# Kernel optimization log

Measured on AMD Instinct MI355X. Metric: run time of the kernel, lower is better.

## Reference

```python
import jax, jax.numpy as jnp
import numpy as np

TMP1 = 0.01
TMP2 = 0.1
TMP3 = 0.1
NEG_MARGIN = 0.1  # referenced in source forward but never set in __init__; fixed here
CLAMP_MAX = 88.0


def setup_inputs() -> dict:
    key = jax.random.key(0)
    scores = jax.random.normal(key, (512, 8192), dtype=jnp.float32)
    k_vals = jnp.array([1, 5, 10], dtype=jnp.int32)
    return {"scores": scores, "k_vals": k_vals, "pos_num": 16}


def reference(scores, k_vals, pos_num):
    # scores: [B, N]; first `pos_num` columns are positives (gt == 1), rest negatives.
    P = pos_num
    K = k_vals.shape[0]
    pos = scores[:, :P]          # [B, P]
    neg = scores[:, P:]          # [B, N-P]

    # pairwise diffs: pos rows and neg rows of the per-sample [N, P] diff matrix
    pos_diff = pos[:, :, None] - pos[:, None, :]                    # [B, P, P]
    neg_diff = neg[:, :, None] - pos[:, None, :] + NEG_MARGIN       # [B, N-P, P]

    # negative rows: soft step via temperature-scaled softplus, two-sided
    neg_term = jnp.where(
        neg_diff >= 0,
        jnp.logaddexp(0.0, neg_diff / TMP2) + 0.1,
        jnp.logaddexp(0.0, neg_diff / TMP1),
    )                                                               # [B, N-P, P]

    # positive rows: hard indicator (detached in source), zero the diagonal
    eye = jnp.eye(P, dtype=scores.dtype)
    pos_term = (pos_diff >= 0).astype(scores.dtype) * (1.0 - eye)   # [B, P, P]

    # soft rank of each positive: 1 + sum over all rows
    rank = 1.0 + pos_term.sum(axis=1) + neg_term.sum(axis=1)        # [B, P]

    # soft recall@k penalty per positive and cutoff
    z = (rank[:, :, None] - k_vals[None, None, :].astype(scores.dtype)) / TMP3
    recall = jnp.logaddexp(0.0, jnp.minimum(z, CLAMP_MAX))          # [B, P, K]

    per_sample = recall.sum(axis=(1, 2)) / (P * K)                  # [B]
    return per_sample.mean()
```

## Files before the change

### kernel.cpp

```cpp
#include <hip/hip_runtime.h>


#define ROWS 512
#define COLS 8192
#define POSN 16
#define NK 3
#define NEGF4 2044
#define BLOCK 512

typedef float f32x4 __attribute__((ext_vector_type(4)));

__global__ __launch_bounds__(BLOCK, 4)
void recall_fused_kernel(const float* __restrict__ scores,
                         const int* __restrict__ k_vals,
                         float* __restrict__ out)
{
    const int row  = blockIdx.x;
    const int tid  = threadIdx.x;
    const int wave = tid >> 6;
    const int lane = tid & 63;
    const float* rowp = scores + (size_t)row * COLS;

    __shared__ float s_pos[POSN];
    __shared__ float s_part[8][POSN];

    if (tid < POSN) s_pos[tid] = rowp[tid];
    __syncthreads();

    const float C10 = 14.4269504089f;
    const float A0  = 1.44269504089f;
    const float LN2 = 0.69314718055994531f;

    float p10[POSN];
#pragma unroll
    for (int j = 0; j < POSN; ++j) p10[j] = s_pos[j] * C10;

    float prod[POSN], accM[POSN];
    int   ncnt[POSN];
#pragma unroll
    for (int j = 0; j < POSN; ++j) { prod[j] = 1.0f; accM[j] = 0.0f; ncnt[j] = 0; }

    const f32x4* negs = reinterpret_cast<const f32x4*>(rowp + POSN);

    f32x4 v[4];
#pragma unroll
    for (int it = 0; it < 4; ++it) {
        int f = it * BLOCK + tid;
        if (it == 3 && f >= NEGF4) f = NEGF4 - 1;
        v[it] = __builtin_nontemporal_load(negs + f);
    }
    if (3 * BLOCK + tid >= NEGF4) {
        v[3].x = -1.0e30f; v[3].y = -1.0e30f; v[3].z = -1.0e30f; v[3].w = -1.0e30f;
    }

#pragma unroll
    for (int it = 0; it < 4; ++it) {
        float a10[4];
        a10[0] = __fmaf_rn(v[it].x, C10, A0);
        a10[1] = __fmaf_rn(v[it].y, C10, A0);
        a10[2] = __fmaf_rn(v[it].z, C10, A0);
        a10[3] = __fmaf_rn(v[it].w, C10, A0);
#pragma unroll
        for (int e = 0; e < 4; ++e) {
#pragma unroll
            for (int j = 0; j < POSN; ++j) {
                const float t   = a10[e] - p10[j];
                const float arg = fminf(-t, 10.0f * t);
                const float u   = exp2f(arg);
                prod[j] = __fmaf_rn(prod[j], u, prod[j]);
                accM[j] += fmaxf(t, 0.0f);
                ncnt[j] += (int)(__float_as_uint(t) >> 31);
            }
        }
    }

#pragma unroll
    for (int j = 0; j < POSN; ++j) {
        const float nge = 16.0f - (float)ncnt[j];
        float s = __fmaf_rn(accM[j] + __log2f(prod[j]), LN2, 0.1f * nge);
#pragma unroll
        for (int off = 32; off > 0; off >>= 1)
            s += __shfl_xor(s, off);
        if (lane == 0) s_part[wave][j] = s;
    }
    __syncthreads();

    if (tid < POSN) {
        const int j = tid;
        float negsum = 0.0f;
#pragma unroll
        for (int w = 0; w < 8; ++w) negsum += s_part[w][j];

        const float pj = s_pos[j];
        float cnt = -1.0f;
#pragma unroll
        for (int i = 0; i < POSN; ++i)
            cnt += (s_pos[i] >= pj) ? 1.0f : 0.0f;

        const float rank = 1.0f + cnt + negsum;

        float rsum = 0.0f;
#pragma unroll
        for (int k = 0; k < NK; ++k) {
            float z = (rank - (float)k_vals[k]) * 10.0f;
            z = fminf(z, 88.0f);
            const float e2 = exp2f(-1.44269504089f * fabsf(z));
            rsum += fmaxf(z, 0.0f) + LN2 * __log2f(1.0f + e2);
        }

        rsum += __shfl_xor(rsum, 8);
        rsum += __shfl_xor(rsum, 4);
        rsum += __shfl_xor(rsum, 2);
        rsum += __shfl_xor(rsum, 1);
        if (j == 0)
            atomicAdd(out, rsum * (1.0f / ((float)POSN * NK * ROWS)));
    }
}

extern "C" void kernel_launch(void* const* d_in, const int* in_sizes, int n_in,
                              void* d_out, int out_size, void* d_ws, size_t ws_size,
                              hipStream_t stream) {
    const float* scores = (const float*)d_in[0];
    const int*   k_vals = (const int*)d_in[1];
    float* out = (float*)d_out;

    hipMemsetAsync(out, 0, sizeof(float), stream);
    recall_fused_kernel<<<ROWS, BLOCK, 0, stream>>>(scores, k_vals, out);
}
```

Baseline: 96.69 us.

## Restructure negative-term inner loop with abs-sum identity, wave ballot counts, raw intrinsics

Rewrites the per-pair inner loop so that max(t,0) is derived from a shared row sum plus a per-positive sum of |t|, using max(t,0) = (t+|t|)/2. The count of non-negative diffs now comes from a wave-level ballot and popcount, and exp2/log use raw AMDGCN intrinsics instead of the libm wrappers. Positives are read straight into registers rather than staged through shared memory, which drops the first barrier, and loads switch to a wave-contiguous index with normal instead of nontemporal loads. The aim is fewer VALU ops per pair, at the cost of ballot traffic per iteration and a padding value of -100 that must keep the out-of-range lanes harmless under the new sum formulation.

Measured after the change: 155.9 us. 1.61x slower.

```diff
diff --git a/kernel.cpp b/kernel.cpp
--- a/kernel.cpp
+++ b/kernel.cpp
@@ -21,37 +21,37 @@
     const int lane = tid & 63;
     const float* rowp = scores + (size_t)row * COLS;
 
-    __shared__ float s_pos[POSN];
-    __shared__ float s_part[8][POSN];
-
-    if (tid < POSN) s_pos[tid] = rowp[tid];
-    __syncthreads();
-
     const float C10 = 14.4269504089f;
     const float A0  = 1.44269504089f;
     const float LN2 = 0.69314718055994531f;
 
-    float p10[POSN];
-#pragma unroll
-    for (int j = 0; j < POSN; ++j) p10[j] = s_pos[j] * C10;
-
-    float prod[POSN], accM[POSN];
-    int   ncnt[POSN];
-#pragma unroll
-    for (int j = 0; j < POSN; ++j) { prod[j] = 1.0f; accM[j] = 0.0f; ncnt[j] = 0; }
+    __shared__ float s_part[8][POSN];
 
     const f32x4* negs = reinterpret_cast<const f32x4*>(rowp + POSN);
 
     f32x4 v[4];
+    bool ok[4];
 #pragma unroll
     for (int it = 0; it < 4; ++it) {
-        int f = it * BLOCK + tid;
-        if (it == 3 && f >= NEGF4) f = NEGF4 - 1;
-        v[it] = __builtin_nontemporal_load(negs + f);
+        const int f = wave * 256 + it * 64 + lane;
+        ok[it] = (f < NEGF4);
+        v[it] = negs[ok[it] ? f : (NEGF4 - 1)];
     }
-    if (3 * BLOCK + tid >= NEGF4) {
-        v[3].x = -1.0e30f; v[3].y = -1.0e30f; v[3].z = -1.0e30f; v[3].w = -1.0e30f;
+#pragma unroll
+    for (int it = 0; it < 4; ++it) {
+        if (!ok[it]) { v[it].x = -100.0f; v[it].y = -100.0f;
+                       v[it].z = -100.0f; v[it].w = -100.0f; }
     }
+
+    float p_s[POSN], p10[POSN];
+#pragma unroll
+    for (int j = 0; j < POSN; ++j) { p_s[j] = rowp[j]; p10[j] = p_s[j] * C10; }
+
+    float prod[POSN], sumabs[POSN];
+    int   nge[POSN];
+    float suma = 0.0f;
+#pragma unroll
+    for (int j = 0; j < POSN; ++j) { prod[j] = 1.0f; sumabs[j] = 0.0f; nge[j] = 0; }
 
 #pragma unroll
     for (int it = 0; it < 4; ++it) {
@@ -60,28 +60,30 @@
         a10[1] = __fmaf_rn(v[it].y, C10, A0);
         a10[2] = __fmaf_rn(v[it].z, C10, A0);
         a10[3] = __fmaf_rn(v[it].w, C10, A0);
+        suma += (a10[0] + a10[1]) + (a10[2] + a10[3]);
 #pragma unroll
         for (int e = 0; e < 4; ++e) {
 #pragma unroll
             for (int j = 0; j < POSN; ++j) {
                 const float t   = a10[e] - p10[j];
                 const float arg = fminf(-t, 10.0f * t);
-                const float u   = exp2f(arg);
-                prod[j] = __fmaf_rn(prod[j], u, prod[j]);
-                accM[j] += fmaxf(t, 0.0f);
-                ncnt[j] += (int)(__float_as_uint(t) >> 31);
+                const float u   = __builtin_amdgcn_exp2f(arg);
+                prod[j]   = __fmaf_rn(prod[j], u, prod[j]);
+                sumabs[j] += fabsf(t);
+                nge[j] += (int)__popcll(__ballot(t >= 0.0f));
             }
         }
     }
 
 #pragma unroll
     for (int j = 0; j < POSN; ++j) {
-        const float nge = 16.0f - (float)ncnt[j];
-        float s = __fmaf_rn(accM[j] + __log2f(prod[j]), LN2, 0.1f * nge);
+        float s = (suma - 16.0f * p10[j] + sumabs[j]) * 0.5f
+                + __builtin_amdgcn_logf(prod[j]);
 #pragma unroll
         for (int off = 32; off > 0; off >>= 1)
             s += __shfl_xor(s, off);
-        if (lane == 0) s_part[wave][j] = s;
+        if (lane == 0)
+            s_part[wave][j] = __fmaf_rn(s, LN2, 0.1f * (float)nge[j]);
     }
     __syncthreads();
 
@@ -91,11 +93,11 @@
 #pragma unroll
         for (int w = 0; w < 8; ++w) negsum += s_part[w][j];
 
-        const float pj = s_pos[j];
+        const float pj = rowp[j];
         float cnt = -1.0f;
 #pragma unroll
         for (int i = 0; i < POSN; ++i)
-            cnt += (s_pos[i] >= pj) ? 1.0f : 0.0f;
+            cnt += (p_s[i] >= pj) ? 1.0f : 0.0f;
 
         const float rank = 1.0f + cnt + negsum;
 
@@ -104,8 +106,8 @@
         for (int k = 0; k < NK; ++k) {
             float z = (rank - (float)k_vals[k]) * 10.0f;
             z = fminf(z, 88.0f);
-            const float e2 = exp2f(-1.44269504089f * fabsf(z));
-            rsum += fmaxf(z, 0.0f) + LN2 * __log2f(1.0f + e2);
+            const float e2 = __builtin_amdgcn_exp2f(-1.44269504089f * fabsf(z));
+            rsum += fmaxf(z, 0.0f) + LN2 * __builtin_amdgcn_logf(1.0f + e2);
         }
 
         rsum += __shfl_xor(rsum, 8);
```
